# Kernel tuning notes

Measured on AMD Instinct MI355X. Metric: run time of the kernel, lower is better.

The kernel has to match this reference:

```python
import jax, jax.numpy as jnp
import numpy as np

BIT_LEN = 64
CGC = (21, 42)
GAP = 16
HID = 1024

def setup_inputs() -> dict:
    key = jax.random.key(0)
    ks = jax.random.split(key, 16)
    B, F = 2048, 4096
    s_fc1 = 0.01  # torch init: normal(0, 0.01) for Linear weights, zero bias
    inp = {
        'x_low': jax.random.normal(ks[0], (B, F), jnp.float32),
        'x_mid': jax.random.normal(ks[1], (B, F), jnp.float32),
        'x_hig': jax.random.normal(ks[2], (B, F), jnp.float32),
        # low/mid/hig MLPs: Linear(F,1024) -> ReLU -> Linear(1024,1024) -> ReLU (dropout = identity in eval)
        'low_W1': jax.random.normal(ks[3], (HID, F), jnp.float32) * s_fc1,
        'low_b1': jnp.zeros((HID,), jnp.float32),
        'low_W2': jax.random.normal(ks[4], (HID, HID), jnp.float32) * s_fc1,
        'low_b2': jnp.zeros((HID,), jnp.float32),
        'mid_W1': jax.random.normal(ks[5], (HID, F), jnp.float32) * s_fc1,
        'mid_b1': jnp.zeros((HID,), jnp.float32),
        'mid_W2': jax.random.normal(ks[6], (HID, HID), jnp.float32) * s_fc1,
        'mid_b2': jnp.zeros((HID,), jnp.float32),
        'hig_W1': jax.random.normal(ks[7], (HID, F), jnp.float32) * s_fc1,
        'hig_b1': jnp.zeros((HID,), jnp.float32),
        'hig_W2': jax.random.normal(ks[8], (HID, HID), jnp.float32) * s_fc1,
        'hig_b2': jnp.zeros((HID,), jnp.float32),
        # RNNCell (tanh) params; torch default uniform(-1/sqrt(H), 1/sqrt(H)); biases filled 0 by the module
        'W_ih': jax.random.uniform(ks[9], (HID, HID), jnp.float32, -1.0, 1.0) / np.sqrt(HID),
        'W_hh': jax.random.uniform(ks[10], (HID, HID), jnp.float32, -1.0, 1.0) / np.sqrt(HID),
        'b_ih': jnp.zeros((HID,), jnp.float32),
        'b_hh': jnp.zeros((HID,), jnp.float32),
        # actor head Linear(1024, 1)
        'W_act': jax.random.normal(ks[11], (1, HID), jnp.float32) * s_fc1,
        'b_act': jnp.zeros((1,), jnp.float32),
    }
    return inp

def _mlp(x, W1, b1, W2, b2):
    h = jax.nn.relu(x @ W1.T + b1)
    return jax.nn.relu(h @ W2.T + b2)

def _cell(x, h, W_ih, W_hh, b_ih, b_hh):
    return jnp.tanh(x @ W_ih.T + b_ih + h @ W_hh.T + b_hh)

def reference(x_low, x_mid, x_hig,
              low_W1, low_b1, low_W2, low_b2,
              mid_W1, mid_b1, mid_W2, mid_b2,
              hig_W1, hig_b1, hig_W2, hig_b2,
              W_ih, W_hh, b_ih, b_hh, W_act, b_act):
    xl = _mlp(x_low, low_W1, low_b1, low_W2, low_b2)
    xm = _mlp(x_mid, mid_W1, mid_b1, mid_W2, mid_b2)
    xh = _mlp(x_hig, hig_W1, hig_b1, hig_W2, hig_b2)
    hx = xh
    ipt = xh
    tip = 1  # static Python counter -> branch structure is compile-time constant
    probs = []
    for step in range(BIT_LEN):
        if step == CGC[0]:
            ipt = xm
            hx = _cell(ipt, hx, W_ih, W_hh, b_ih, b_hh)
            tip = 1
        elif step == CGC[1]:
            ipt = xl
            hx = _cell(ipt, hx, W_ih, W_hh, b_ih, b_hh)
            tip = 1
        elif tip % GAP == 0:
            hx = _cell(ipt, hx, W_ih, W_hh, b_ih, b_hh)
            tip = 1
        else:
            hx = _cell(hx, hx, W_ih, W_hh, b_ih, b_hh)
            tip = tip + 1
        probs.append(jax.nn.sigmoid(hx @ W_act.T + b_act))  # [B, 1]
    return jnp.stack(probs), hx  # [bit_len, B, 1], [B, 1024]
```

## Files before the change

### kernel.cpp

```cpp
#include <hip/hip_runtime.h>
#include <hip/hip_bf16.h>

typedef unsigned short u16;
typedef short bf16x8 __attribute__((ext_vector_type(8)));
typedef float floatx4 __attribute__((ext_vector_type(4)));

#define B_DIM 2048
#define F_DIM 4096
#define H_DIM 1024
#define NSTEP 64

__device__ __forceinline__ float fast_tanh(float x) {
    return 1.0f - 2.0f / (__expf(2.0f * x) + 1.0f);
}

__device__ __forceinline__ u16 f2b(float x) {
    union { __hip_bfloat16 b; u16 u; } v;
    v.b = __float2bfloat16(x);
    return v.u;
}

__device__ __forceinline__ void ldg16_dev(int4& d, const void* p) {
    asm volatile("global_load_dwordx4 %0, %1, off sc0 sc1" : "=v"(d) : "v"(p));
}
__device__ __forceinline__ void ldg16(int4& d, const void* p) {
    asm volatile("global_load_dwordx4 %0, %1, off" : "=v"(d) : "v"(p));
}
__device__ __forceinline__ void stg2_dev(void* p, unsigned v) {
    asm volatile("global_store_short %0, %1, off sc0 sc1" :: "v"(p), "v"(v) : "memory");
}
#define VMEM_DRAIN() do { asm volatile("s_waitcnt vmcnt(0)" ::: "memory"); \
                          __builtin_amdgcn_sched_barrier(0); } while (0)

template<int F32>
__device__ __forceinline__ int4 ld8(const void* base, size_t elemOff) {
    if constexpr (F32) {
        const float* p = (const float*)base + elemOff;
        float4 lo = *(const float4*)p;
        float4 hi = *(const float4*)(p + 4);
        union { u16 h[8]; int4 v; } rr;
        rr.h[0] = f2b(lo.x); rr.h[1] = f2b(lo.y); rr.h[2] = f2b(lo.z); rr.h[3] = f2b(lo.w);
        rr.h[4] = f2b(hi.x); rr.h[5] = f2b(hi.y); rr.h[6] = f2b(hi.z); rr.h[7] = f2b(hi.w);
        return rr.v;
    } else {
        return *(const int4*)((const u16*)base + elemOff);
    }
}

template<int AF32, int WF32, int ACT, int OUT_F32>
__global__ __launch_bounds__(256)
void gemm64(const void* __restrict__ A0, const void* __restrict__ A1, const void* __restrict__ A2,
            const void* __restrict__ Wp0, const void* __restrict__ Wp1, const void* __restrict__ Wp2,
            const float* __restrict__ bia0, const float* __restrict__ bia1, const float* __restrict__ bia2,
            void* __restrict__ C0, void* __restrict__ C1, void* __restrict__ C2,
            const int N, const int K)
{
    constexpr int BM = 64, BN = 64, BK = 64, LS = 72;
    __shared__ u16 As[2][BM * LS];
    __shared__ u16 Bs[2][BN * LS];

    const int z = blockIdx.z;
    const void*  A     = (z == 0) ? A0 : (z == 1) ? A1 : A2;
    const void*  W     = (z == 0) ? Wp0 : (z == 1) ? Wp1 : Wp2;
    const float* bias1 = (z == 0) ? bia0 : (z == 1) ? bia1 : bia2;
    void*        Cout  = (z == 0) ? C0 : (z == 1) ? C1 : C2;

    const int tid  = threadIdx.x;
    const int wave = tid >> 6, lane = tid & 63;
    const int wm = wave >> 1, wn = wave & 1;
    const int r = lane & 15, q = lane >> 4;

    const int lin = blockIdx.y * 16 + blockIdx.x;
    const int mti = (lin & 7) | ((lin >> 7) << 3);
    const int nti = (lin >> 3) & 15;
    const int m0 = mti * BM, n0 = nti * BN;

    floatx4 acc[2][2];
    const floatx4 zf = {0.f, 0.f, 0.f, 0.f};
    #pragma unroll
    for (int a = 0; a < 2; a++)
        #pragma unroll
        for (int b = 0; b < 2; b++) acc[a][b] = zf;

    const int row0 = tid >> 3, kc = (tid & 7) << 3, row1 = row0 + 32;
    const size_t aOff0 = (size_t)(m0 + row0) * K + kc;
    const size_t aOff1 = (size_t)(m0 + row1) * K + kc;
    const size_t wOff0 = (size_t)(n0 + row0) * K + kc;
    const size_t wOff1 = (size_t)(n0 + row1) * K + kc;

    int4 av0 = ld8<AF32>(A, aOff0);
    int4 av1 = ld8<AF32>(A, aOff1);
    int4 bv0 = ld8<WF32>(W, wOff0);
    int4 bv1 = ld8<WF32>(W, wOff1);

    int p = 0;
    for (int kb = 0; kb < K; kb += BK) {
        *(int4*)&As[p][row0 * LS + kc] = av0;
        *(int4*)&As[p][row1 * LS + kc] = av1;
        *(int4*)&Bs[p][row0 * LS + kc] = bv0;
        *(int4*)&Bs[p][row1 * LS + kc] = bv1;
        __syncthreads();
        if (kb + BK < K) {
            av0 = ld8<AF32>(A, aOff0 + kb + BK);
            av1 = ld8<AF32>(A, aOff1 + kb + BK);
            bv0 = ld8<WF32>(W, wOff0 + kb + BK);
            bv1 = ld8<WF32>(W, wOff1 + kb + BK);
        }
        bf16x8 af[2][2], bfr[2][2];
        #pragma unroll
        for (int ks = 0; ks < 2; ks++)
            #pragma unroll
            for (int t = 0; t < 2; t++) {
                af[ks][t]  = *(const bf16x8*)&As[p][(wm * 32 + t * 16 + r) * LS + ks * 32 + q * 8];
                bfr[ks][t] = *(const bf16x8*)&Bs[p][(wn * 32 + t * 16 + r) * LS + ks * 32 + q * 8];
            }
        #pragma unroll
        for (int ks = 0; ks < 2; ks++)
            #pragma unroll
            for (int mt = 0; mt < 2; mt++)
                #pragma unroll
                for (int nt = 0; nt < 2; nt++)
                    acc[mt][nt] = __builtin_amdgcn_mfma_f32_16x16x32_bf16(af[ks][mt], bfr[ks][nt], acc[mt][nt], 0, 0, 0);
        p ^= 1;
    }

    #pragma unroll
    for (int mt = 0; mt < 2; mt++)
        #pragma unroll
        for (int nt = 0; nt < 2; nt++) {
            const int col  = n0 + wn * 32 + nt * 16 + r;
            const int rowb = m0 + wm * 32 + mt * 16 + q * 4;
            const float bb = bias1 ? bias1[col] : 0.f;
            #pragma unroll
            for (int i = 0; i < 4; i++) {
                float v = acc[mt][nt][i] + bb;
                if (ACT == 1) v = fmaxf(v, 0.f);
                if (OUT_F32) ((float*)Cout)[(size_t)(rowb + i) * N + col] = v;
                else ((u16*)Cout)[(size_t)(rowb + i) * N + col] = f2b(v);
            }
        }
}

__global__ __launch_bounds__(256, 2)
void rnn_persist(u16* __restrict__ bufA, u16* __restrict__ bufB,
                 const u16* __restrict__ Wsum, const u16* __restrict__ Whhb,
                 const float* __restrict__ bsum, const float* __restrict__ bhh,
                 const float* __restrict__ pre_xh, const float* __restrict__ pre_xm,
                 const float* __restrict__ pre_xl,
                 const float* __restrict__ Wact, float* __restrict__ logits,
                 float* __restrict__ outHx, unsigned* __restrict__ gsync)
{
    constexpr int BM = 64, BN = 64, BK = 128, K = H_DIM, N = H_DIM;
    __shared__ u16 As[2][BM * BK];
    __shared__ u16 Bs[2][BN * BK];

    const int tid  = threadIdx.x;
    const int wave = tid >> 6, lane = tid & 63;
    const int wm = wave >> 1, wn = wave & 1;
    const int r = lane & 15, q = lane >> 4;

    const int lin = blockIdx.x;
    const int mti = (lin & 7) | ((lin >> 7) << 3);
    const int nti = (lin >> 3) & 15;
    const int m0 = mti * BM, n0 = nti * BN;

    const int row = tid >> 2, c = tid & 3;
    const size_t aOff = (size_t)(m0 + row) * K + c * 8;
    const size_t wOff = (size_t)(n0 + row) * K + c * 8;
    int dst[4];
    #pragma unroll
    for (int j = 0; j < 4; j++)
        dst[j] = row * BK + (((c * 8) + j * 32) ^ ((row & 7) * 8));
    const int sw = (r & 7) * 8;

    unsigned* cnt = gsync + mti * 32;

    const u16* cur = bufA;
    u16* nxt = bufB;

    for (int s = 0; s < NSTEP; ++s) {
        const u16* W; const float* bias; const float* pre = nullptr;
        if (s == 15)                 { W = Whhb; bias = bhh; pre = pre_xh; }
        else if (s == 21 || s == 37) { W = Whhb; bias = bhh; pre = pre_xm; }
        else if (s == 42 || s == 58) { W = Whhb; bias = bhh; pre = pre_xl; }
        else                         { W = Wsum; bias = bsum; }
        const bool last = (s == NSTEP - 1);

        floatx4 acc[2][2];
        const floatx4 zf = {0.f, 0.f, 0.f, 0.f};
        acc[0][0] = zf; acc[0][1] = zf; acc[1][0] = zf; acc[1][1] = zf;

        int4 av[4], bv[4];
        #pragma unroll
        for (int j = 0; j < 4; j++) {
            ldg16_dev(av[j], cur + aOff + j * 32);
            ldg16(bv[j], W + wOff + j * 32);
        }

        int p = 0;
        for (int kb = 0; kb < K; kb += BK) {
            VMEM_DRAIN();
            #pragma unroll
            for (int j = 0; j < 4; j++) {
                *(int4*)&As[p][dst[j]] = av[j];
                *(int4*)&Bs[p][dst[j]] = bv[j];
            }
            __syncthreads();
            if (kb + BK < K) {
                #pragma unroll
                for (int j = 0; j < 4; j++) {
                    ldg16_dev(av[j], cur + aOff + kb + BK + j * 32);
                    ldg16(bv[j], W + wOff + kb + BK + j * 32);
                }
            }
            #pragma unroll
            for (int ks = 0; ks < 4; ks++) {
                const int cb = ((ks * 32) + q * 8) ^ sw;
                bf16x8 a0 = *(const bf16x8*)&As[p][(wm * 32 +      r) * BK + cb];
                bf16x8 a1 = *(const bf16x8*)&As[p][(wm * 32 + 16 + r) * BK + cb];
                bf16x8 b0 = *(const bf16x8*)&Bs[p][(wn * 32 +      r) * BK + cb];
                bf16x8 b1 = *(const bf16x8*)&Bs[p][(wn * 32 + 16 + r) * BK + cb];
                acc[0][0] = __builtin_amdgcn_mfma_f32_16x16x32_bf16(a0, b0, acc[0][0], 0, 0, 0);
                acc[0][1] = __builtin_amdgcn_mfma_f32_16x16x32_bf16(a0, b1, acc[0][1], 0, 0, 0);
                acc[1][0] = __builtin_amdgcn_mfma_f32_16x16x32_bf16(a1, b0, acc[1][0], 0, 0, 0);
                acc[1][1] = __builtin_amdgcn_mfma_f32_16x16x32_bf16(a1, b1, acc[1][1], 0, 0, 0);
            }
            p ^= 1;
        }

        const int col0 = n0 + wn * 32 + r;
        const int col1 = col0 + 16;
        const float bb0 = bias[col0], bb1 = bias[col1];
        const float wa0 = Wact[col0], wa1 = Wact[col1];
        #pragma unroll
        for (int mt = 0; mt < 2; mt++) {
            const int rowb = m0 + wm * 32 + mt * 16 + q * 4;
            #pragma unroll
            for (int i = 0; i < 4; i++) {
                float v0 = acc[mt][0][i] + bb0;
                float v1 = acc[mt][1][i] + bb1;
                if (pre) {
                    v0 += pre[(size_t)(rowb + i) * N + col0];
                    v1 += pre[(size_t)(rowb + i) * N + col1];
                }
                v0 = fast_tanh(v0);
                v1 = fast_tanh(v1);
                if (last) {
                    outHx[(size_t)(rowb + i) * N + col0] = v0;
                    outHx[(size_t)(rowb + i) * N + col1] = v1;
                } else {
                    stg2_dev(nxt + (size_t)(rowb + i) * N + col0, (unsigned)f2b(v0));
                    stg2_dev(nxt + (size_t)(rowb + i) * N + col1, (unsigned)f2b(v1));
                }
                acc[mt][0][i] = v0;
                acc[mt][1][i] = v1;
            }
        }

        VMEM_DRAIN();
        __syncthreads();
        float* sc = (float*)As;
        #pragma unroll
        for (int mt = 0; mt < 2; mt++)
            #pragma unroll
            for (int i = 0; i < 4; i++) {
                float v = acc[mt][0][i] * wa0 + acc[mt][1][i] * wa1;
                v += __shfl_xor(v, 1);
                v += __shfl_xor(v, 2);
                v += __shfl_xor(v, 4);
                v += __shfl_xor(v, 8);
                if (r == 0) sc[wn * 64 + wm * 32 + mt * 16 + q * 4 + i] = v;
            }
        __syncthreads();
        if (tid < 64) {
            float v = sc[tid] + sc[64 + tid];
            atomicAdd(&logits[(size_t)s * B_DIM + m0 + tid], v);
        }

        if (!last) {
            if (tid == 0) {
                __hip_atomic_fetch_add(cnt, 1u, __ATOMIC_RELAXED, __HIP_MEMORY_SCOPE_AGENT);
                const unsigned tgt = 16u * (unsigned)(s + 1);
                while (__hip_atomic_load(cnt, __ATOMIC_RELAXED, __HIP_MEMORY_SCOPE_AGENT) < tgt)
                    __builtin_amdgcn_s_sleep(2);
            }
            __syncthreads();
            const u16* t = cur; cur = nxt; nxt = (u16*)t;
        }
    }
}

__global__ void prep_w(const float* __restrict__ Wih, const float* __restrict__ Whh,
                       u16* __restrict__ Wsum, u16* __restrict__ Whhb, u16* __restrict__ Wihb,
                       const float* __restrict__ bih, const float* __restrict__ bhh,
                       float* __restrict__ bsum, int n) {
    int i = blockIdx.x * 256 + threadIdx.x;
    if (i < n) {
        float a = Wih[i], b = Whh[i];
        Wsum[i] = f2b(a + b);
        Whhb[i] = f2b(b);
        Wihb[i] = f2b(a);
    }
    if (i < H_DIM) bsum[i] = bih[i] + bhh[i];
}

__global__ void sigmoid_kernel(const float* __restrict__ logits, const float* __restrict__ b_act,
                               float* __restrict__ out, int n) {
    int i = blockIdx.x * 256 + threadIdx.x;
    if (i < n) {
        float zv = logits[i] + b_act[0];
        out[i] = 1.0f / (1.0f + __expf(-zv));
    }
}

extern "C" void kernel_launch(void* const* d_in, const int* in_sizes, int n_in,
                              void* d_out, int out_size, void* d_ws, size_t ws_size,
                              hipStream_t stream) {
    (void)in_sizes; (void)n_in; (void)out_size; (void)ws_size;
    const int Bn = B_DIM, F = F_DIM, H = H_DIM;

    const float* xin[3] = {(const float*)d_in[0], (const float*)d_in[1], (const float*)d_in[2]};
    const float* W1[3]  = {(const float*)d_in[3], (const float*)d_in[7], (const float*)d_in[11]};
    const float* b1[3]  = {(const float*)d_in[4], (const float*)d_in[8], (const float*)d_in[12]};
    const float* W2[3]  = {(const float*)d_in[5], (const float*)d_in[9], (const float*)d_in[13]};
    const float* b2[3]  = {(const float*)d_in[6], (const float*)d_in[10], (const float*)d_in[14]};
    const float* W_ih   = (const float*)d_in[15];
    const float* W_hh   = (const float*)d_in[16];
    const float* b_ih   = (const float*)d_in[17];
    const float* b_hh   = (const float*)d_in[18];
    const float* W_act  = (const float*)d_in[19];
    const float* b_act  = (const float*)d_in[20];

    const size_t MB = 1024 * 1024;
    char* ws = (char*)d_ws;
    u16*   xl     = (u16*)(ws + 0 * MB);
    u16*   xm     = (u16*)(ws + 4 * MB);
    u16*   xh     = (u16*)(ws + 8 * MB);
    u16*   hxB    = (u16*)(ws + 12 * MB);
    u16*   Wsum   = (u16*)(ws + 16 * MB);
    u16*   Whhb   = (u16*)(ws + 18 * MB);
    u16*   Wihb   = (u16*)(ws + 20 * MB);
    u16*   h1a    = (u16*)(ws + 22 * MB);
    u16*   h1b    = (u16*)(ws + 26 * MB);
    u16*   h1c    = (u16*)(ws + 30 * MB);
    float* pre_xh = (float*)(ws + 22 * MB);
    float* pre_xm = (float*)(ws + 30 * MB);
    float* pre_xl = (float*)(ws + 38 * MB);
    float* logits = (float*)(ws + 46 * MB);
    float* bsum   = (float*)(ws + 46 * MB + 512 * 1024);
    unsigned* gsync = (unsigned*)(ws + 46 * MB + 516 * 1024);

    dim3 blk(256);
    dim3 grid3(16, 32, 3);

    (void)hipMemsetAsync(logits, 0, (size_t)NSTEP * Bn * sizeof(float), stream);
    (void)hipMemsetAsync(gsync, 0, 4096, stream);
    prep_w<<<dim3((H * H + 255) / 256), blk, 0, stream>>>(W_ih, W_hh, Wsum, Whhb, Wihb,
                                                          b_ih, b_hh, bsum, H * H);

    u16* h1[3] = {h1a, h1b, h1c};
    gemm64<1,1,1,0><<<grid3, blk, 0, stream>>>(
        xin[0], xin[1], xin[2], W1[0], W1[1], W1[2], b1[0], b1[1], b1[2],
        h1[0], h1[1], h1[2], H, F);
    gemm64<0,1,1,0><<<grid3, blk, 0, stream>>>(
        h1a, h1b, h1c, W2[0], W2[1], W2[2], b2[0], b2[1], b2[2],
        xl, xm, xh, H, H);
    gemm64<0,0,0,1><<<grid3, blk, 0, stream>>>(
        xh, xm, xl, Wihb, Wihb, Wihb, b_ih, b_ih, b_ih,
        pre_xh, pre_xm, pre_xl, H, H);

    float* outHx = (float*)d_out + (size_t)NSTEP * Bn;
    rnn_persist<<<dim3(512), dim3(256), 0, stream>>>(
        xh, hxB, Wsum, Whhb, bsum, b_hh, pre_xh, pre_xm, pre_xl,
        W_act, logits, outHx, gsync);

    sigmoid_kernel<<<dim3((NSTEP * Bn + 255) / 256), blk, 0, stream>>>(
        logits, b_act, (float*)d_out, NSTEP * Bn);
}
```

Baseline: 1.338 ms.

## Deepen RNN load pipeline, coalesce hidden-state stores, pre-convert MLP inputs to bf16

The persistent RNN kernel now keeps two K-tiles of global loads in flight, using partial vmcnt waits instead of a full drain before each tile. It stages the bf16 tanh output in shared memory and writes it back as 16-byte coalesced stores instead of scattered 2-byte stores, and signals the step counter right after those stores land, before the logits atomics. When the workspace is large enough, the MLP inputs and weights are first converted to bf16 by separate kernels, so the GEMMs read bf16 rather than converting fp32 inside the tile loads. The costs are more registers, extra conversion passes and extra workspace memory.

```diff
diff --git a/kernel.cpp b/kernel.cpp
--- a/kernel.cpp
+++ b/kernel.cpp
@@ -4,6 +4,7 @@
 typedef unsigned short u16;
 typedef short bf16x8 __attribute__((ext_vector_type(8)));
 typedef float floatx4 __attribute__((ext_vector_type(4)));
+typedef int   intx4  __attribute__((ext_vector_type(4)));
 
 #define B_DIM 2048
 #define F_DIM 4096
@@ -26,8 +27,9 @@
 __device__ __forceinline__ void ldg16(int4& d, const void* p) {
     asm volatile("global_load_dwordx4 %0, %1, off" : "=v"(d) : "v"(p));
 }
-__device__ __forceinline__ void stg2_dev(void* p, unsigned v) {
-    asm volatile("global_store_short %0, %1, off sc0 sc1" :: "v"(p), "v"(v) : "memory");
+__device__ __forceinline__ void stg16_dev(void* p, intx4 v) {
+    asm volatile("global_store_dwordx4 %0, %1, off sc0 sc1"
+                 :: "v"(p), "v"(v) : "memory");
 }
 #define VMEM_DRAIN() do { asm volatile("s_waitcnt vmcnt(0)" ::: "memory"); \
                           __builtin_amdgcn_sched_barrier(0); } while (0)
@@ -150,7 +152,7 @@
                  const float* __restrict__ Wact, float* __restrict__ logits,
                  float* __restrict__ outHx, unsigned* __restrict__ gsync)
 {
-    constexpr int BM = 64, BN = 64, BK = 128, K = H_DIM, N = H_DIM;
+    constexpr int BM = 64, BN = 64, BK = 128, K = H_DIM, N = H_DIM, NITER = K / BK;
     __shared__ u16 As[2][BM * BK];
     __shared__ u16 Bs[2][BN * BK];
 
@@ -190,27 +192,38 @@
         const floatx4 zf = {0.f, 0.f, 0.f, 0.f};
         acc[0][0] = zf; acc[0][1] = zf; acc[1][0] = zf; acc[1][1] = zf;
 
-        int4 av[4], bv[4];
+        int4 av0[4], bv0[4], av1[4], bv1[4];
         #pragma unroll
         for (int j = 0; j < 4; j++) {
-            ldg16_dev(av[j], cur + aOff + j * 32);
-            ldg16(bv[j], W + wOff + j * 32);
+            ldg16_dev(av0[j], cur + aOff + j * 32);
+            ldg16(bv0[j], W + wOff + j * 32);
+        }
+        #pragma unroll
+        for (int j = 0; j < 4; j++) {
+            ldg16_dev(av1[j], cur + aOff + BK + j * 32);
+            ldg16(bv1[j], W + wOff + BK + j * 32);
         }
 
         int p = 0;
-        for (int kb = 0; kb < K; kb += BK) {
-            VMEM_DRAIN();
+        #pragma unroll
+        for (int it = 0; it < NITER; ++it) {
+            if (it < NITER - 1) { asm volatile("s_waitcnt vmcnt(8)" ::: "memory"); }
+            else                { asm volatile("s_waitcnt vmcnt(0)" ::: "memory"); }
+            __builtin_amdgcn_sched_barrier(0);
+            int4 (&av)[4] = (it & 1) ? av1 : av0;
+            int4 (&bv)[4] = (it & 1) ? bv1 : bv0;
             #pragma unroll
             for (int j = 0; j < 4; j++) {
                 *(int4*)&As[p][dst[j]] = av[j];
                 *(int4*)&Bs[p][dst[j]] = bv[j];
             }
             __syncthreads();
-            if (kb + BK < K) {
+            if (it + 2 < NITER) {
+                const int kb2 = (it + 2) * BK;
                 #pragma unroll
                 for (int j = 0; j < 4; j++) {
-                    ldg16_dev(av[j], cur + aOff + kb + BK + j * 32);
-                    ldg16(bv[j], W + wOff + kb + BK + j * 32);
+                    ldg16_dev(av[j], cur + aOff + kb2 + j * 32);
+                    ldg16(bv[j], W + wOff + kb2 + j * 32);
                 }
             }
             #pragma unroll
@@ -232,6 +245,7 @@
         const int col1 = col0 + 16;
         const float bb0 = bias[col0], bb1 = bias[col1];
         const float wa0 = Wact[col0], wa1 = Wact[col1];
+        float fv0[2][4], fv1[2][4];
         #pragma unroll
         for (int mt = 0; mt < 2; mt++) {
             const int rowb = m0 + wm * 32 + mt * 16 + q * 4;
@@ -243,28 +257,41 @@
                     v0 += pre[(size_t)(rowb + i) * N + col0];
                     v1 += pre[(size_t)(rowb + i) * N + col1];
                 }
-                v0 = fast_tanh(v0);
-                v1 = fast_tanh(v1);
-                if (last) {
-                    outHx[(size_t)(rowb + i) * N + col0] = v0;
-                    outHx[(size_t)(rowb + i) * N + col1] = v1;
-                } else {
-                    stg2_dev(nxt + (size_t)(rowb + i) * N + col0, (unsigned)f2b(v0));
-                    stg2_dev(nxt + (size_t)(rowb + i) * N + col1, (unsigned)f2b(v1));
+                fv0[mt][i] = fast_tanh(v0);
+                fv1[mt][i] = fast_tanh(v1);
+            }
+        }
+        if (last) {
+            #pragma unroll
+            for (int mt = 0; mt < 2; mt++) {
+                const int rowb = m0 + wm * 32 + mt * 16 + q * 4;
+                #pragma unroll
+                for (int i = 0; i < 4; i++) {
+                    outHx[(size_t)(rowb + i) * N + col0] = fv0[mt][i];
+                    outHx[(size_t)(rowb + i) * N + col1] = fv1[mt][i];
                 }
-                acc[mt][0][i] = v0;
-                acc[mt][1][i] = v1;
-            }
-        }
-
-        VMEM_DRAIN();
+            }
+        }
+
         __syncthreads();
-        float* sc = (float*)As;
+        u16*   Cs = (u16*)As;
+        float* sc = (float*)((char*)As + 8192);
+        if (!last) {
+            #pragma unroll
+            for (int mt = 0; mt < 2; mt++) {
+                const int rl = wm * 32 + mt * 16 + q * 4;
+                #pragma unroll
+                for (int i = 0; i < 4; i++) {
+                    Cs[(rl + i) * 64 + wn * 32 + r]      = f2b(fv0[mt][i]);
+                    Cs[(rl + i) * 64 + wn * 32 + 16 + r] = f2b(fv1[mt][i]);
+                }
+            }
+        }
         #pragma unroll
         for (int mt = 0; mt < 2; mt++)
             #pragma unroll
             for (int i = 0; i < 4; i++) {
-                float v = acc[mt][0][i] * wa0 + acc[mt][1][i] * wa1;
+                float v = fv0[mt][i] * wa0 + fv1[mt][i] * wa1;
                 v += __shfl_xor(v, 1);
                 v += __shfl_xor(v, 2);
                 v += __shfl_xor(v, 4);
@@ -272,14 +299,26 @@
                 if (r == 0) sc[wn * 64 + wm * 32 + mt * 16 + q * 4 + i] = v;
             }
         __syncthreads();
+
+        if (!last) {
+            #pragma unroll
+            for (int u2 = 0; u2 < 2; u2++) {
+                const int ch = tid + u2 * 256;
+                const int rw = ch >> 3, cc = ch & 7;
+                intx4 val = *(const intx4*)&Cs[rw * 64 + cc * 8];
+                stg16_dev(nxt + (size_t)(m0 + rw) * N + n0 + cc * 8, val);
+            }
+            VMEM_DRAIN();
+            if (tid == 0)
+                __hip_atomic_fetch_add(cnt, 1u, __ATOMIC_RELAXED, __HIP_MEMORY_SCOPE_AGENT);
+        }
         if (tid < 64) {
             float v = sc[tid] + sc[64 + tid];
             atomicAdd(&logits[(size_t)s * B_DIM + m0 + tid], v);
         }
-
         if (!last) {
+            VMEM_DRAIN();
             if (tid == 0) {
-                __hip_atomic_fetch_add(cnt, 1u, __ATOMIC_RELAXED, __HIP_MEMORY_SCOPE_AGENT);
                 const unsigned tgt = 16u * (unsigned)(s + 1);
                 while (__hip_atomic_load(cnt, __ATOMIC_RELAXED, __HIP_MEMORY_SCOPE_AGENT) < tgt)
                     __builtin_amdgcn_s_sleep(2);
@@ -287,6 +326,25 @@
             __syncthreads();
             const u16* t = cur; cur = nxt; nxt = (u16*)t;
         }
+    }
+}
+
+__global__ void convert_bf16(const float* __restrict__ s0, const float* __restrict__ s1,
+                             const float* __restrict__ s2,
+                             u16* __restrict__ d0, u16* __restrict__ d1, u16* __restrict__ d2,
+                             int n)
+{
+    const int z = blockIdx.z;
+    const float* s = (z == 0) ? s0 : (z == 1) ? s1 : s2;
+    u16* d = (z == 0) ? d0 : (z == 1) ? d1 : d2;
+    int i = (blockIdx.x * 256 + threadIdx.x) * 8;
+    if (i < n) {
+        float4 lo = *(const float4*)(s + i);
+        float4 hi = *(const float4*)(s + i + 4);
+        union { u16 h[8]; int4 v; } rr;
+        rr.h[0] = f2b(lo.x); rr.h[1] = f2b(lo.y); rr.h[2] = f2b(lo.z); rr.h[3] = f2b(lo.w);
+        rr.h[4] = f2b(hi.x); rr.h[5] = f2b(hi.y); rr.h[6] = f2b(hi.z); rr.h[7] = f2b(hi.w);
+        *(int4*)(d + i) = rr.v;
     }
 }
 
@@ -316,7 +374,7 @@
 extern "C" void kernel_launch(void* const* d_in, const int* in_sizes, int n_in,
                               void* d_out, int out_size, void* d_ws, size_t ws_size,
                               hipStream_t stream) {
-    (void)in_sizes; (void)n_in; (void)out_size; (void)ws_size;
+    (void)in_sizes; (void)n_in; (void)out_size;
     const int Bn = B_DIM, F = F_DIM, H = H_DIM;
 
     const float* xin[3] = {(const float*)d_in[0], (const float*)d_in[1], (const float*)d_in[2]};
@@ -349,6 +407,10 @@
     float* logits = (float*)(ws + 46 * MB);
     float* bsum   = (float*)(ws + 46 * MB + 512 * 1024);
     unsigned* gsync = (unsigned*)(ws + 46 * MB + 516 * 1024);
+    u16* xb[3]  = {(u16*)(ws + 48 * MB), (u16*)(ws + 64 * MB), (u16*)(ws + 80 * MB)};
+    u16* W1b[3] = {(u16*)(ws + 96 * MB), (u16*)(ws + 104 * MB), (u16*)(ws + 112 * MB)};
+    u16* W2b[3] = {(u16*)(ws + 120 * MB), (u16*)(ws + 122 * MB), (u16*)(ws + 124 * MB)};
+    const bool big = ws_size >= (size_t)126 * MB;
 
     dim3 blk(256);
     dim3 grid3(16, 32, 3);
@@ -359,12 +421,28 @@
                                                           b_ih, b_hh, bsum, H * H);
 
     u16* h1[3] = {h1a, h1b, h1c};
-    gemm64<1,1,1,0><<<grid3, blk, 0, stream>>>(
-        xin[0], xin[1], xin[2], W1[0], W1[1], W1[2], b1[0], b1[1], b1[2],
-        h1[0], h1[1], h1[2], H, F);
-    gemm64<0,1,1,0><<<grid3, blk, 0, stream>>>(
-        h1a, h1b, h1c, W2[0], W2[1], W2[2], b2[0], b2[1], b2[2],
-        xl, xm, xh, H, H);
+    if (big) {
+        const int nX = Bn * F, nW1 = H * F, nW2 = H * H;
+        convert_bf16<<<dim3((nX / 8 + 255) / 256, 1, 3), blk, 0, stream>>>(
+            xin[0], xin[1], xin[2], xb[0], xb[1], xb[2], nX);
+        convert_bf16<<<dim3((nW1 / 8 + 255) / 256, 1, 3), blk, 0, stream>>>(
+            W1[0], W1[1], W1[2], W1b[0], W1b[1], W1b[2], nW1);
+        convert_bf16<<<dim3((nW2 / 8 + 255) / 256, 1, 3), blk, 0, stream>>>(
+            W2[0], W2[1], W2[2], W2b[0], W2b[1], W2b[2], nW2);
+        gemm64<0,0,1,0><<<grid3, blk, 0, stream>>>(
+            xb[0], xb[1], xb[2], W1b[0], W1b[1], W1b[2], b1[0], b1[1], b1[2],
+            h1[0], h1[1], h1[2], H, F);
+        gemm64<0,0,1,0><<<grid3, blk, 0, stream>>>(
+            h1a, h1b, h1c, W2b[0], W2b[1], W2b[2], b2[0], b2[1], b2[2],
+            xl, xm, xh, H, H);
+    } else {
+        gemm64<1,1,1,0><<<grid3, blk, 0, stream>>>(
+            xin[0], xin[1], xin[2], W1[0], W1[1], W1[2], b1[0], b1[1], b1[2],
+            h1[0], h1[1], h1[2], H, F);
+        gemm64<0,1,1,0><<<grid3, blk, 0, stream>>>(
+            h1a, h1b, h1c, W2[0], W2[1], W2[2], b2[0], b2[1], b2[2],
+            xl, xm, xh, H, H);
+    }
     gemm64<0,0,0,1><<<grid3, blk, 0, stream>>>(
         xh, xm, xl, Wihb, Wihb, Wihb, b_ih, b_ih, b_ih,
         pre_xh, pre_xm, pre_xl, H, H);
```

Result: faster. 1.188 ms (-11.2%).
